# Performance work log

Measured on AMD Instinct MI355X. Metric: run time of the kernel, lower is better.

Reference implementation:

```python
import jax, jax.numpy as jnp
import numpy as np
import math

H = 16
D_MODEL = 1024
D_K = D_MODEL // H  # 64
B = 4
S = 2048
D_V = 64


def setup_inputs() -> dict:
    key0 = jax.random.key(0)
    ks = jax.random.split(key0, 7)
    scale = 1.0 / math.sqrt(D_MODEL)
    return {
        "query": jax.random.normal(ks[0], (B, S, D_MODEL), jnp.float32),
        "key": jax.random.normal(ks[1], (B, S, D_MODEL), jnp.float32),
        "value": jax.random.normal(ks[2], (B, D_V, S), jnp.float32),
        "Wq": jax.random.normal(ks[3], (D_MODEL, D_MODEL), jnp.float32) * scale,
        "bq": jax.random.normal(ks[4], (D_MODEL,), jnp.float32) * scale,
        "Wk": jax.random.normal(ks[5], (D_MODEL, D_MODEL), jnp.float32) * scale,
        "bk": jax.random.normal(ks[6], (D_MODEL,), jnp.float32) * scale,
    }


def reference(query, key, value, Wq, bq, Wk, bk):
    nb = query.shape[0]
    # Linear projections then split heads: [B,S,d_model] -> [B,h,S,d_k]
    q = (query @ Wq.T + bq).reshape(nb, -1, H, D_K).transpose(0, 2, 1, 3)
    k = (key @ Wk.T + bk).reshape(nb, -1, H, D_K).transpose(0, 2, 1, 3)
    # value.repeat(h,1,1,1).permute(1,0,3,2): [B,dv,Sk] -> broadcast over heads
    # with last two axes swapped -> effectively v[b,s,d] = value[b,d,s]
    v = jnp.swapaxes(value, 1, 2)  # [B, Sk, dv]
    # Scaled dot-product attention (mask branch is a no-op: m == zeros)
    scores = jnp.einsum("bhqd,bhkd->bhqk", q, k) / math.sqrt(D_K)
    p_attn = jax.nn.softmax(scores, axis=-1)
    # value identical across heads, contract directly with base v
    x = jnp.einsum("bhqk,bkd->bhqd", p_attn, v)  # [B,h,Sq,dv]
    return (jnp.mean(x, axis=1), q)
```

## Files before the change

### kernel.cpp

```cpp
#include <hip/hip_runtime.h>


typedef unsigned short u16;
typedef __attribute__((ext_vector_type(8))) u16 u16x8;
typedef __attribute__((ext_vector_type(8))) __bf16 bf16x8;
typedef __attribute__((ext_vector_type(4))) float f32x4;
typedef __attribute__((ext_vector_type(16))) float f32x16;
typedef __attribute__((ext_vector_type(2))) unsigned u32x2;
typedef __attribute__((ext_vector_type(4))) unsigned u32x4;

typedef const __attribute__((address_space(1))) void gvoid;
typedef __attribute__((address_space(3))) void lvoid;

__device__ __forceinline__ void gload16(const void* g, void* l) {
  __builtin_amdgcn_global_load_lds((gvoid*)g, (lvoid*)l, 16, 0, 0);
}

__device__ __forceinline__ u16 f2bf(float f) {
  unsigned u = __builtin_bit_cast(unsigned, f);
  u += 0x7fffu + ((u >> 16) & 1u);
  return (u16)(u >> 16);
}

__device__ __forceinline__ unsigned cvtpk(float lo, float hi) {
  unsigned r;
  asm("v_cvt_pk_bf16_f32 %0, %1, %2" : "=v"(r) : "v"(lo), "v"(hi));
  return r;
}

__device__ __forceinline__ float exp2a(float x) {
  float r;
  asm("v_exp_f32 %0, %1" : "=v"(r) : "v"(x));
  return r;
}

__device__ __forceinline__ f32x16 zero16() {
  f32x16 z;
#pragma unroll
  for (int i = 0; i < 16; ++i) z[i] = 0.f;
  return z;
}

__global__ void cvt_small(const float* __restrict__ wq, const float* __restrict__ wk,
                          const float* __restrict__ v,
                          u16* __restrict__ wqb, u16* __restrict__ wkb, u16* __restrict__ vb) {
  int i = blockIdx.x * 256 + threadIdx.x;
  const float* s;
  u16* d;
  int off;
  if (i < 262144)      { s = wq; d = wqb; off = i; }
  else if (i < 524288) { s = wk; d = wkb; off = i - 262144; }
  else if (i < 655360) { s = v;  d = vb;  off = i - 524288; }
  else return;
  float4 x = reinterpret_cast<const float4*>(s)[off];
  ushort4 o;
  o.x = f2bf(x.x); o.y = f2bf(x.y); o.z = f2bf(x.z); o.w = f2bf(x.w);
  reinterpret_cast<ushort4*>(d)[off] = o;
}

__global__ __launch_bounds__(256) void proj_gemm(
    const float* __restrict__ qf, const float* __restrict__ kf,
    const u16* __restrict__ Wqb, const u16* __restrict__ Wkb,
    const float* __restrict__ bq, const float* __restrict__ bk,
    float* __restrict__ out1, u16* __restrict__ k_ws)
{
  const int z = blockIdx.z;
  const float* __restrict__ A = z ? kf : qf;
  const u16* __restrict__ W = z ? Wkb : Wqb;
  const float* __restrict__ bias = z ? bk : bq;

  __shared__ u16 As[128 * 64];
  __shared__ u16 Bs[128 * 64];

  const int tid = threadIdx.x;
  const int lane = tid & 63;
  const int w = tid >> 6;
  const int ln = lane & 15;
  const int lh = lane >> 4;
  const int wm = w >> 1, wn = w & 1;
  const int n0 = blockIdx.x * 128;
  const int j0 = blockIdx.y * 128;

  f32x4 acc[4][4];
#pragma unroll
  for (int mt = 0; mt < 4; ++mt)
#pragma unroll
    for (int nt = 0; nt < 4; ++nt)
      acc[mt][nt] = f32x4{0.f, 0.f, 0.f, 0.f};

  const int r_ = tid >> 3, c8_ = tid & 7;

  for (int kt = 0; kt < 16; ++kt) {
    __syncthreads();
#pragma unroll
    for (int it = 0; it < 4; ++it) {
      int r = it * 32 + r_;
      gload16(&W[(size_t)(j0 + r) * 1024 + kt * 64 + c8_ * 8], &Bs[(it * 256 + w * 64) * 8]);
    }
#pragma unroll
    for (int j = 0; j < 4; ++j) {
      int u = tid + j * 256;
      int r = u >> 3, c8 = (u & 7) * 8;
      const float* s = &A[(size_t)(n0 + r) * 1024 + kt * 64 + c8];
      float4 x0 = *reinterpret_cast<const float4*>(s);
      float4 x1 = *reinterpret_cast<const float4*>(s + 4);
      u32x4 wv{cvtpk(x0.x, x0.y), cvtpk(x0.z, x0.w), cvtpk(x1.x, x1.y), cvtpk(x1.z, x1.w)};
      *reinterpret_cast<u32x4*>(&As[r * 64 + c8]) = wv;
    }
    __syncthreads();
#pragma unroll
    for (int ks = 0; ks < 2; ++ks) {
      bf16x8 a[4], bfr[4];
#pragma unroll
      for (int mt = 0; mt < 4; ++mt)
        a[mt] = __builtin_bit_cast(bf16x8,
            *reinterpret_cast<const u16x8*>(&As[(wm * 64 + mt * 16 + ln) * 64 + lh * 8 + ks * 32]));
#pragma unroll
      for (int nt = 0; nt < 4; ++nt)
        bfr[nt] = __builtin_bit_cast(bf16x8,
            *reinterpret_cast<const u16x8*>(&Bs[(wn * 64 + nt * 16 + ln) * 64 + lh * 8 + ks * 32]));
      __builtin_amdgcn_s_setprio(1);
#pragma unroll
      for (int mt = 0; mt < 4; ++mt)
#pragma unroll
        for (int nt = 0; nt < 4; ++nt)
          acc[mt][nt] = __builtin_amdgcn_mfma_f32_16x16x32_bf16(a[mt], bfr[nt], acc[mt][nt], 0, 0, 0);
      __builtin_amdgcn_s_setprio(0);
    }
  }

#pragma unroll
  for (int nt = 0; nt < 4; ++nt) {
    int j = j0 + wn * 64 + nt * 16 + ln;
    float bv = bias[j];
    int h = j >> 6, d = j & 63;
#pragma unroll
    for (int mt = 0; mt < 4; ++mt) {
#pragma unroll
      for (int r = 0; r < 4; ++r) {
        int n = n0 + wm * 64 + mt * 16 + lh * 4 + r;
        int bidx = n >> 11, s = n & 2047;
        size_t off = ((size_t)(bidx * 16 + h) * 2048 + s) * 64 + d;
        float val = acc[mt][nt][r] + bv;
        if (z == 0) out1[off] = val;
        else        k_ws[off] = f2bf(val);
      }
    }
  }
}

__global__ __launch_bounds__(256) void attn_kernel(
    const float* __restrict__ qf, const u16* __restrict__ k_ws,
    const u16* __restrict__ valb, float* __restrict__ x_ws)
{
  const int wgid = (blockIdx.x & 7) * 128 + (blockIdx.x >> 3);
  const int qblk = wgid & 15;
  const int h = (wgid >> 4) & 15;
  const int b = wgid >> 8;
  const int bh = b * 16 + h;

  const int tid = threadIdx.x, lane = tid & 63, w = tid >> 6;
  const int l31 = lane & 31, hi = lane >> 5;
  const int xm = (lane & 7) << 4;

  __shared__ u16 Kt[2][4096];
  __shared__ u16 Vt[2][4096];
  char* KtB = (char*)&Kt[0][0];
  char* VtB = (char*)&Vt[0][0];

  bf16x8 aq[4];
  {
    const float qs = 0.125f * 1.4426950408889634f;
    const size_t qbase = ((size_t)bh * 2048 + qblk * 128 + w * 32 + l31) * 64;
#pragma unroll
    for (int c = 0; c < 4; ++c) {
      float4 v0 = *reinterpret_cast<const float4*>(&qf[qbase + c * 16 + hi * 8]);
      float4 v1 = *reinterpret_cast<const float4*>(&qf[qbase + c * 16 + hi * 8 + 4]);
      u16x8 t;
      t[0] = f2bf(v0.x * qs); t[1] = f2bf(v0.y * qs);
      t[2] = f2bf(v0.z * qs); t[3] = f2bf(v0.w * qs);
      t[4] = f2bf(v1.x * qs); t[5] = f2bf(v1.y * qs);
      t[6] = f2bf(v1.z * qs); t[7] = f2bf(v1.w * qs);
      aq[c] = __builtin_bit_cast(bf16x8, t);
    }
  }

  const u16* kg = k_ws + (size_t)bh * 131072;
  const u16* vg = valb + (size_t)b * 131072;
  const int u0 = tid, u1 = tid + 256;
  const u16* ks0 = kg + (u0 >> 3) * 64 + ((u0 ^ (u0 >> 3)) & 7) * 8;
  const u16* ks1 = kg + (u1 >> 3) * 64 + ((u1 ^ (u1 >> 3)) & 7) * 8;
  const u16* vs0 = vg + (u0 >> 3) * 2048 + ((u0 ^ (u0 >> 3)) & 7) * 8;
  const u16* vs1 = vg + (u1 >> 3) * 2048 + ((u1 ^ (u1 >> 3)) & 7) * 8;
  u16* kd0 = &Kt[0][(w * 64) * 8];
  u16* kd1 = &Kt[0][(256 + w * 64) * 8];
  u16* vd0 = &Vt[0][(w * 64) * 8];
  u16* vd1 = &Vt[0][(256 + w * 64) * 8];

  gload16(ks0, kd0); gload16(ks1, kd1);
  gload16(vs0, vd0); gload16(vs1, vd1);

  float l_loc = 0.0f;
  f32x16 oA = zero16(), oB = zero16();
  int cur = 0;
  __syncthreads();

  for (int t = 0; t < 32; ++t) {
    if (t < 31) {
      int nb = (cur ^ 1) * 4096;
      size_t ko = (size_t)(t + 1) * 4096;
      int vo = (t + 1) * 64;
      gload16(ks0 + ko, kd0 + nb); gload16(ks1 + ko, kd1 + nb);
      gload16(vs0 + vo, vd0 + nb); gload16(vs1 + vo, vd1 + nb);
    }
    const int bo = cur * 8192;

#pragma unroll
    for (int st = 0; st < 2; ++st) {
      f32x16 p = zero16();
      __builtin_amdgcn_s_setprio(1);
#pragma unroll
      for (int c = 0; c < 4; ++c) {
        int kaddr = bo + ((((st * 32 + l31) * 128) + c * 32 + hi * 16) ^ xm);
        bf16x8 kf = __builtin_bit_cast(bf16x8, *reinterpret_cast<const u16x8*>(KtB + kaddr));
        p = __builtin_amdgcn_mfma_f32_32x32x16_bf16(kf, aq[c], p, 0, 0, 0);
      }
      __builtin_amdgcn_s_setprio(0);

#pragma unroll
      for (int r = 0; r < 16; ++r) p[r] = exp2a(p[r]);
      float s0 = (p[0] + p[1]) + (p[2] + p[3]);
      float s1 = (p[4] + p[5]) + (p[6] + p[7]);
      float s2 = (p[8] + p[9]) + (p[10] + p[11]);
      float s3 = (p[12] + p[13]) + (p[14] + p[15]);
      l_loc += (s0 + s1) + (s2 + s3);

      u32x2 sA0 = __builtin_amdgcn_permlane32_swap(cvtpk(p[0], p[1]),   cvtpk(p[4], p[5]),   false, false);
      u32x2 sB0 = __builtin_amdgcn_permlane32_swap(cvtpk(p[2], p[3]),   cvtpk(p[6], p[7]),   false, false);
      u32x2 sA1 = __builtin_amdgcn_permlane32_swap(cvtpk(p[8], p[9]),   cvtpk(p[12], p[13]), false, false);
      u32x2 sB1 = __builtin_amdgcn_permlane32_swap(cvtpk(p[10], p[11]), cvtpk(p[14], p[15]), false, false);
      u32x4 w0{sA0[0], sB0[0], sA0[1], sB0[1]};
      u32x4 w1{sA1[0], sB1[0], sA1[1], sB1[1]};
      bf16x8 pf0 = __builtin_bit_cast(bf16x8, w0);
      bf16x8 pf1 = __builtin_bit_cast(bf16x8, w1);

#pragma unroll
      for (int kc = 0; kc < 2; ++kc) {
        bf16x8 pf = kc ? pf1 : pf0;
        int cb = st * 64 + kc * 32 + hi * 16;
        bf16x8 vA = __builtin_bit_cast(bf16x8,
            *reinterpret_cast<const u16x8*>(VtB + bo + ((l31 * 128 + cb) ^ xm)));
        bf16x8 vB = __builtin_bit_cast(bf16x8,
            *reinterpret_cast<const u16x8*>(VtB + bo + (((32 + l31) * 128 + cb) ^ xm)));
        __builtin_amdgcn_s_setprio(1);
        oA = __builtin_amdgcn_mfma_f32_32x32x16_bf16(vA, pf, oA, 0, 0, 0);
        oB = __builtin_amdgcn_mfma_f32_32x32x16_bf16(vB, pf, oB, 0, 0, 0);
        __builtin_amdgcn_s_setprio(0);
      }
    }
    __syncthreads();
    cur ^= 1;
  }

  float l_run = l_loc + __shfl_xor(l_loc, 32);
  float inv = 1.0f / l_run;
  size_t obase = ((size_t)bh * 2048 + qblk * 128 + w * 32 + l31) * 64;
#pragma unroll
  for (int g = 0; g < 4; ++g) {
    float4 aa, bb;
    aa.x = oA[g * 4 + 0] * inv; aa.y = oA[g * 4 + 1] * inv;
    aa.z = oA[g * 4 + 2] * inv; aa.w = oA[g * 4 + 3] * inv;
    bb.x = oB[g * 4 + 0] * inv; bb.y = oB[g * 4 + 1] * inv;
    bb.z = oB[g * 4 + 2] * inv; bb.w = oB[g * 4 + 3] * inv;
    *reinterpret_cast<float4*>(&x_ws[obase + g * 8 + hi * 4]) = aa;
    *reinterpret_cast<float4*>(&x_ws[obase + 32 + g * 8 + hi * 4]) = bb;
  }
}

__global__ void mean_heads(const float* __restrict__ x_ws, float* __restrict__ out0) {
  int idx = blockIdx.x * 256 + threadIdx.x;
  int b = idx >> 17;
  int rem = idx & 131071;
  float s = 0.f;
#pragma unroll
  for (int h = 0; h < 16; ++h) s += x_ws[((size_t)(b * 16 + h) << 17) + rem];
  out0[idx] = s * 0.0625f;
}

extern "C" void kernel_launch(void* const* d_in, const int* in_sizes, int n_in,
                              void* d_out, int out_size, void* d_ws, size_t ws_size,
                              hipStream_t stream) {
  (void)in_sizes; (void)n_in; (void)out_size; (void)ws_size;
  const float* query = (const float*)d_in[0];
  const float* key   = (const float*)d_in[1];
  const float* value = (const float*)d_in[2];
  const float* Wq    = (const float*)d_in[3];
  const float* bq    = (const float*)d_in[4];
  const float* Wk    = (const float*)d_in[5];
  const float* bk    = (const float*)d_in[6];

  float* out0 = (float*)d_out;
  float* out1 = out0 + 524288;

  char* ws = (char*)d_ws;
  const size_t MB = 1u << 20;
  u16* Wqb  = (u16*)(ws + 32 * MB);
  u16* Wkb  = (u16*)(ws + 34 * MB);
  u16* valb = (u16*)(ws + 36 * MB);
  u16* k_ws = (u16*)(ws + 37 * MB);
  float* x_ws = (float*)(ws + 0);

  cvt_small<<<2560, 256, 0, stream>>>(Wq, Wk, value, Wqb, Wkb, valb);
  proj_gemm<<<dim3(64, 8, 2), 256, 0, stream>>>(query, key, Wqb, Wkb, bq, bk, out1, k_ws);
  attn_kernel<<<1024, 256, 0, stream>>>(out1, k_ws, valb, x_ws);
  mean_heads<<<2048, 256, 0, stream>>>(x_ws, out0);
}
```

Baseline: 175.0 us.

## Double attention workgroup to 512 threads with 256 queries sharing each K/V tile

The attention kernel now launches 512 workgroups of 8 waves, each covering 256 query rows, so every K/V tile staged in LDS is reused by twice as many waves. Each thread issues one async global-to-LDS load per tensor instead of two. The inner loop also computes both QK^T score tiles before running the softmax and PV MMAs, giving the scheduler more independent work. The cost is fewer workgroups, register pressure from holding two score tiles under the 512-thread launch bound, and barriers that now synchronise twice as many waves.

```diff
diff --git a/kernel.cpp b/kernel.cpp
--- a/kernel.cpp
+++ b/kernel.cpp
@@ -149,14 +149,30 @@
   }
 }
 
-__global__ __launch_bounds__(256) void attn_kernel(
+#define SOFTMAX_CVT(P, PF0, PF1)                                                     \
+  {                                                                                  \
+    _Pragma("unroll")                                                                \
+    for (int r = 0; r < 16; ++r) P[r] = exp2a(P[r]);                                 \
+    l_loc += (((P[0]+P[1])+(P[2]+P[3])) + ((P[4]+P[5])+(P[6]+P[7])))                 \
+           + (((P[8]+P[9])+(P[10]+P[11])) + ((P[12]+P[13])+(P[14]+P[15])));          \
+    u32x2 sA0 = __builtin_amdgcn_permlane32_swap(cvtpk(P[0],P[1]),   cvtpk(P[4],P[5]),   false,false); \
+    u32x2 sB0 = __builtin_amdgcn_permlane32_swap(cvtpk(P[2],P[3]),   cvtpk(P[6],P[7]),   false,false); \
+    u32x2 sA1 = __builtin_amdgcn_permlane32_swap(cvtpk(P[8],P[9]),   cvtpk(P[12],P[13]), false,false); \
+    u32x2 sB1 = __builtin_amdgcn_permlane32_swap(cvtpk(P[10],P[11]), cvtpk(P[14],P[15]), false,false); \
+    u32x4 w0_{sA0[0], sB0[0], sA0[1], sB0[1]};                                       \
+    u32x4 w1_{sA1[0], sB1[0], sA1[1], sB1[1]};                                       \
+    PF0 = __builtin_bit_cast(bf16x8, w0_);                                           \
+    PF1 = __builtin_bit_cast(bf16x8, w1_);                                           \
+  }
+
+__global__ __launch_bounds__(512) void attn_kernel(
     const float* __restrict__ qf, const u16* __restrict__ k_ws,
     const u16* __restrict__ valb, float* __restrict__ x_ws)
 {
-  const int wgid = (blockIdx.x & 7) * 128 + (blockIdx.x >> 3);
-  const int qblk = wgid & 15;
-  const int h = (wgid >> 4) & 15;
-  const int b = wgid >> 8;
+  const int wgid = (blockIdx.x & 7) * 64 + (blockIdx.x >> 3);
+  const int qblk = wgid & 7;
+  const int h = (wgid >> 3) & 15;
+  const int b = wgid >> 7;
   const int bh = b * 16 + h;
 
   const int tid = threadIdx.x, lane = tid & 63, w = tid >> 6;
@@ -171,7 +187,7 @@
   bf16x8 aq[4];
   {
     const float qs = 0.125f * 1.4426950408889634f;
-    const size_t qbase = ((size_t)bh * 2048 + qblk * 128 + w * 32 + l31) * 64;
+    const size_t qbase = ((size_t)bh * 2048 + qblk * 256 + w * 32 + l31) * 64;
 #pragma unroll
     for (int c = 0; c < 4; ++c) {
       float4 v0 = *reinterpret_cast<const float4*>(&qf[qbase + c * 16 + hi * 8]);
@@ -187,18 +203,13 @@
 
   const u16* kg = k_ws + (size_t)bh * 131072;
   const u16* vg = valb + (size_t)b * 131072;
-  const int u0 = tid, u1 = tid + 256;
-  const u16* ks0 = kg + (u0 >> 3) * 64 + ((u0 ^ (u0 >> 3)) & 7) * 8;
-  const u16* ks1 = kg + (u1 >> 3) * 64 + ((u1 ^ (u1 >> 3)) & 7) * 8;
-  const u16* vs0 = vg + (u0 >> 3) * 2048 + ((u0 ^ (u0 >> 3)) & 7) * 8;
-  const u16* vs1 = vg + (u1 >> 3) * 2048 + ((u1 ^ (u1 >> 3)) & 7) * 8;
-  u16* kd0 = &Kt[0][(w * 64) * 8];
-  u16* kd1 = &Kt[0][(256 + w * 64) * 8];
-  u16* vd0 = &Vt[0][(w * 64) * 8];
-  u16* vd1 = &Vt[0][(256 + w * 64) * 8];
-
-  gload16(ks0, kd0); gload16(ks1, kd1);
-  gload16(vs0, vd0); gload16(vs1, vd1);
+  const u16* ksA = kg + (tid >> 3) * 64 + ((tid ^ (tid >> 3)) & 7) * 8;
+  const u16* vsA = vg + (tid >> 3) * 2048 + ((tid ^ (tid >> 3)) & 7) * 8;
+  u16* kdA = &Kt[0][w * 512];
+  u16* vdA = &Vt[0][w * 512];
+
+  gload16(ksA, kdA);
+  gload16(vsA, vdA);
 
   float l_loc = 0.0f;
   f32x16 oA = zero16(), oB = zero16();
@@ -208,63 +219,73 @@
   for (int t = 0; t < 32; ++t) {
     if (t < 31) {
       int nb = (cur ^ 1) * 4096;
-      size_t ko = (size_t)(t + 1) * 4096;
-      int vo = (t + 1) * 64;
-      gload16(ks0 + ko, kd0 + nb); gload16(ks1 + ko, kd1 + nb);
-      gload16(vs0 + vo, vd0 + nb); gload16(vs1 + vo, vd1 + nb);
+      gload16(ksA + (size_t)(t + 1) * 4096, kdA + nb);
+      gload16(vsA + (t + 1) * 64, vdA + nb);
     }
     const int bo = cur * 8192;
 
-#pragma unroll
-    for (int st = 0; st < 2; ++st) {
-      f32x16 p = zero16();
+    f32x16 p0 = zero16(), p1 = zero16();
+    __builtin_amdgcn_s_setprio(1);
+#pragma unroll
+    for (int c = 0; c < 4; ++c) {
+      int ka = bo + (((l31 * 128) + c * 32 + hi * 16) ^ xm);
+      bf16x8 kf = __builtin_bit_cast(bf16x8, *reinterpret_cast<const u16x8*>(KtB + ka));
+      p0 = __builtin_amdgcn_mfma_f32_32x32x16_bf16(kf, aq[c], p0, 0, 0, 0);
+    }
+#pragma unroll
+    for (int c = 0; c < 4; ++c) {
+      int ka = bo + ((((32 + l31) * 128) + c * 32 + hi * 16) ^ xm);
+      bf16x8 kf = __builtin_bit_cast(bf16x8, *reinterpret_cast<const u16x8*>(KtB + ka));
+      p1 = __builtin_amdgcn_mfma_f32_32x32x16_bf16(kf, aq[c], p1, 0, 0, 0);
+    }
+    __builtin_amdgcn_s_setprio(0);
+
+    bf16x8 pf00, pf01, pf10, pf11;
+    SOFTMAX_CVT(p0, pf00, pf01);
+
+    {
+      bf16x8 vA0 = __builtin_bit_cast(bf16x8,
+          *reinterpret_cast<const u16x8*>(VtB + bo + ((l31 * 128 + 0 * 32 + hi * 16) ^ xm)));
+      bf16x8 vB0 = __builtin_bit_cast(bf16x8,
+          *reinterpret_cast<const u16x8*>(VtB + bo + (((32 + l31) * 128 + 0 * 32 + hi * 16) ^ xm)));
+      bf16x8 vA1 = __builtin_bit_cast(bf16x8,
+          *reinterpret_cast<const u16x8*>(VtB + bo + ((l31 * 128 + 1 * 32 + hi * 16) ^ xm)));
+      bf16x8 vB1 = __builtin_bit_cast(bf16x8,
+          *reinterpret_cast<const u16x8*>(VtB + bo + (((32 + l31) * 128 + 1 * 32 + hi * 16) ^ xm)));
       __builtin_amdgcn_s_setprio(1);
-#pragma unroll
-      for (int c = 0; c < 4; ++c) {
-        int kaddr = bo + ((((st * 32 + l31) * 128) + c * 32 + hi * 16) ^ xm);
-        bf16x8 kf = __builtin_bit_cast(bf16x8, *reinterpret_cast<const u16x8*>(KtB + kaddr));
-        p = __builtin_amdgcn_mfma_f32_32x32x16_bf16(kf, aq[c], p, 0, 0, 0);
-      }
+      oA = __builtin_amdgcn_mfma_f32_32x32x16_bf16(vA0, pf00, oA, 0, 0, 0);
+      oB = __builtin_amdgcn_mfma_f32_32x32x16_bf16(vB0, pf00, oB, 0, 0, 0);
+      oA = __builtin_amdgcn_mfma_f32_32x32x16_bf16(vA1, pf01, oA, 0, 0, 0);
+      oB = __builtin_amdgcn_mfma_f32_32x32x16_bf16(vB1, pf01, oB, 0, 0, 0);
       __builtin_amdgcn_s_setprio(0);
-
-#pragma unroll
-      for (int r = 0; r < 16; ++r) p[r] = exp2a(p[r]);
-      float s0 = (p[0] + p[1]) + (p[2] + p[3]);
-      float s1 = (p[4] + p[5]) + (p[6] + p[7]);
-      float s2 = (p[8] + p[9]) + (p[10] + p[11]);
-      float s3 = (p[12] + p[13]) + (p[14] + p[15]);
-      l_loc += (s0 + s1) + (s2 + s3);
-
-      u32x2 sA0 = __builtin_amdgcn_permlane32_swap(cvtpk(p[0], p[1]),   cvtpk(p[4], p[5]),   false, false);
-      u32x2 sB0 = __builtin_amdgcn_permlane32_swap(cvtpk(p[2], p[3]),   cvtpk(p[6], p[7]),   false, false);
-      u32x2 sA1 = __builtin_amdgcn_permlane32_swap(cvtpk(p[8], p[9]),   cvtpk(p[12], p[13]), false, false);
-      u32x2 sB1 = __builtin_amdgcn_permlane32_swap(cvtpk(p[10], p[11]), cvtpk(p[14], p[15]), false, false);
-      u32x4 w0{sA0[0], sB0[0], sA0[1], sB0[1]};
-      u32x4 w1{sA1[0], sB1[0], sA1[1], sB1[1]};
-      bf16x8 pf0 = __builtin_bit_cast(bf16x8, w0);
-      bf16x8 pf1 = __builtin_bit_cast(bf16x8, w1);
-
-#pragma unroll
-      for (int kc = 0; kc < 2; ++kc) {
-        bf16x8 pf = kc ? pf1 : pf0;
-        int cb = st * 64 + kc * 32 + hi * 16;
-        bf16x8 vA = __builtin_bit_cast(bf16x8,
-            *reinterpret_cast<const u16x8*>(VtB + bo + ((l31 * 128 + cb) ^ xm)));
-        bf16x8 vB = __builtin_bit_cast(bf16x8,
-            *reinterpret_cast<const u16x8*>(VtB + bo + (((32 + l31) * 128 + cb) ^ xm)));
-        __builtin_amdgcn_s_setprio(1);
-        oA = __builtin_amdgcn_mfma_f32_32x32x16_bf16(vA, pf, oA, 0, 0, 0);
-        oB = __builtin_amdgcn_mfma_f32_32x32x16_bf16(vB, pf, oB, 0, 0, 0);
-        __builtin_amdgcn_s_setprio(0);
-      }
-    }
+    }
+
+    SOFTMAX_CVT(p1, pf10, pf11);
+
+    {
+      bf16x8 vA0 = __builtin_bit_cast(bf16x8,
+          *reinterpret_cast<const u16x8*>(VtB + bo + ((l31 * 128 + 64 + 0 * 32 + hi * 16) ^ xm)));
+      bf16x8 vB0 = __builtin_bit_cast(bf16x8,
+          *reinterpret_cast<const u16x8*>(VtB + bo + (((32 + l31) * 128 + 64 + 0 * 32 + hi * 16) ^ xm)));
+      bf16x8 vA1 = __builtin_bit_cast(bf16x8,
+          *reinterpret_cast<const u16x8*>(VtB + bo + ((l31 * 128 + 64 + 1 * 32 + hi * 16) ^ xm)));
+      bf16x8 vB1 = __builtin_bit_cast(bf16x8,
+          *reinterpret_cast<const u16x8*>(VtB + bo + (((32 + l31) * 128 + 64 + 1 * 32 + hi * 16) ^ xm)));
+      __builtin_amdgcn_s_setprio(1);
+      oA = __builtin_amdgcn_mfma_f32_32x32x16_bf16(vA0, pf10, oA, 0, 0, 0);
+      oB = __builtin_amdgcn_mfma_f32_32x32x16_bf16(vB0, pf10, oB, 0, 0, 0);
+      oA = __builtin_amdgcn_mfma_f32_32x32x16_bf16(vA1, pf11, oA, 0, 0, 0);
+      oB = __builtin_amdgcn_mfma_f32_32x32x16_bf16(vB1, pf11, oB, 0, 0, 0);
+      __builtin_amdgcn_s_setprio(0);
+    }
+
     __syncthreads();
     cur ^= 1;
   }
 
   float l_run = l_loc + __shfl_xor(l_loc, 32);
   float inv = 1.0f / l_run;
-  size_t obase = ((size_t)bh * 2048 + qblk * 128 + w * 32 + l31) * 64;
+  size_t obase = ((size_t)bh * 2048 + qblk * 256 + w * 32 + l31) * 64;
 #pragma unroll
   for (int g = 0; g < 4; ++g) {
     float4 aa, bb;
@@ -312,6 +333,6 @@
 
   cvt_small<<<2560, 256, 0, stream>>>(Wq, Wk, value, Wqb, Wkb, valb);
   proj_gemm<<<dim3(64, 8, 2), 256, 0, stream>>>(query, key, Wqb, Wkb, bq, bk, out1, k_ws);
-  attn_kernel<<<1024, 256, 0, stream>>>(out1, k_ws, valb, x_ws);
+  attn_kernel<<<512, 512, 0, stream>>>(out1, k_ws, valb, x_ws);
   mean_heads<<<2048, 256, 0, stream>>>(x_ws, out0);
 }
```

After: 173.0 us. About the same (-1.1%).

## Double query rows per wave in attention and store bf16 head outputs

Applied to the files above, without the earlier changes.

Each wave now processes 64 query rows as two 32-row groups, so every K and V fragment read from LDS feeds two MFMAs. This halves the LDS traffic and K/V tile loads per query row, and the attention grid shrinks to 512 blocks. The per-head attention output is now stored as bf16 instead of fp32, and mean_heads reads 8-wide vectors, cutting workspace traffic. The costs are more registers for the doubled accumulators, fewer workgroups to spread across CUs, and lower precision in the intermediate head outputs.

```diff
diff --git a/kernel.cpp b/kernel.cpp
--- a/kernel.cpp
+++ b/kernel.cpp
@@ -149,14 +149,63 @@
   }
 }
 
+#define SOFTMAX_CVT(P, PF0, PF1, LACC)                                               \
+  {                                                                                  \
+    _Pragma("unroll")                                                                \
+    for (int r = 0; r < 16; ++r) P[r] = exp2a(P[r]);                                 \
+    LACC += (((P[0]+P[1])+(P[2]+P[3])) + ((P[4]+P[5])+(P[6]+P[7])))                  \
+          + (((P[8]+P[9])+(P[10]+P[11])) + ((P[12]+P[13])+(P[14]+P[15])));           \
+    u32x2 sA0 = __builtin_amdgcn_permlane32_swap(cvtpk(P[0],P[1]),   cvtpk(P[4],P[5]),   false,false); \
+    u32x2 sB0 = __builtin_amdgcn_permlane32_swap(cvtpk(P[2],P[3]),   cvtpk(P[6],P[7]),   false,false); \
+    u32x2 sA1 = __builtin_amdgcn_permlane32_swap(cvtpk(P[8],P[9]),   cvtpk(P[12],P[13]), false,false); \
+    u32x2 sB1 = __builtin_amdgcn_permlane32_swap(cvtpk(P[10],P[11]), cvtpk(P[14],P[15]), false,false); \
+    u32x4 w0_{sA0[0], sB0[0], sA0[1], sB0[1]};                                       \
+    u32x4 w1_{sA1[0], sB1[0], sA1[1], sB1[1]};                                       \
+    PF0 = __builtin_bit_cast(bf16x8, w0_);                                           \
+    PF1 = __builtin_bit_cast(bf16x8, w1_);                                           \
+  }
+
+#define ST_BLOCK(ST)                                                                 \
+  {                                                                                  \
+    f32x16 pA = zero16(), pB = zero16();                                             \
+    __builtin_amdgcn_s_setprio(1);                                                   \
+    _Pragma("unroll")                                                                \
+    for (int c = 0; c < 4; ++c) {                                                    \
+      int ka = bo + ((((ST * 32 + l31) * 128) + c * 32 + hi * 16) ^ xm);             \
+      bf16x8 kf = __builtin_bit_cast(bf16x8, *reinterpret_cast<const u16x8*>(KtB + ka)); \
+      pA = __builtin_amdgcn_mfma_f32_32x32x16_bf16(kf, aqA[c], pA, 0, 0, 0);         \
+      pB = __builtin_amdgcn_mfma_f32_32x32x16_bf16(kf, aqB[c], pB, 0, 0, 0);         \
+    }                                                                                \
+    __builtin_amdgcn_s_setprio(0);                                                   \
+    bf16x8 fA0, fA1, fB0, fB1;                                                       \
+    SOFTMAX_CVT(pA, fA0, fA1, lA);                                                   \
+    SOFTMAX_CVT(pB, fB0, fB1, lB);                                                   \
+    _Pragma("unroll")                                                                \
+    for (int kc = 0; kc < 2; ++kc) {                                                 \
+      int cb = ST * 64 + kc * 32 + hi * 16;                                          \
+      bf16x8 vA = __builtin_bit_cast(bf16x8,                                         \
+          *reinterpret_cast<const u16x8*>(VtB + bo + ((l31 * 128 + cb) ^ xm)));      \
+      bf16x8 vB = __builtin_bit_cast(bf16x8,                                         \
+          *reinterpret_cast<const u16x8*>(VtB + bo + (((32 + l31) * 128 + cb) ^ xm))); \
+      bf16x8 fA = kc ? fA1 : fA0;                                                    \
+      bf16x8 fB = kc ? fB1 : fB0;                                                    \
+      __builtin_amdgcn_s_setprio(1);                                                 \
+      oA0 = __builtin_amdgcn_mfma_f32_32x32x16_bf16(vA, fA, oA0, 0, 0, 0);           \
+      oB0 = __builtin_amdgcn_mfma_f32_32x32x16_bf16(vB, fA, oB0, 0, 0, 0);           \
+      oA1 = __builtin_amdgcn_mfma_f32_32x32x16_bf16(vA, fB, oA1, 0, 0, 0);           \
+      oB1 = __builtin_amdgcn_mfma_f32_32x32x16_bf16(vB, fB, oB1, 0, 0, 0);           \
+      __builtin_amdgcn_s_setprio(0);                                                 \
+    }                                                                                \
+  }
+
 __global__ __launch_bounds__(256) void attn_kernel(
     const float* __restrict__ qf, const u16* __restrict__ k_ws,
-    const u16* __restrict__ valb, float* __restrict__ x_ws)
+    const u16* __restrict__ valb, u16* __restrict__ x_ws)
 {
-  const int wgid = (blockIdx.x & 7) * 128 + (blockIdx.x >> 3);
-  const int qblk = wgid & 15;
-  const int h = (wgid >> 4) & 15;
-  const int b = wgid >> 8;
+  const int wgid = (blockIdx.x & 7) * 64 + (blockIdx.x >> 3);
+  const int qblk = wgid & 7;
+  const int h = (wgid >> 3) & 15;
+  const int b = wgid >> 7;
   const int bh = b * 16 + h;
 
   const int tid = threadIdx.x, lane = tid & 63, w = tid >> 6;
@@ -168,20 +217,26 @@
   char* KtB = (char*)&Kt[0][0];
   char* VtB = (char*)&Vt[0][0];
 
-  bf16x8 aq[4];
+  bf16x8 aqA[4], aqB[4];
   {
     const float qs = 0.125f * 1.4426950408889634f;
-    const size_t qbase = ((size_t)bh * 2048 + qblk * 128 + w * 32 + l31) * 64;
+    const size_t qb0 = ((size_t)bh * 2048 + qblk * 256 + w * 64 + l31) * 64;
+    const size_t qb1 = qb0 + (size_t)32 * 64;
 #pragma unroll
     for (int c = 0; c < 4; ++c) {
-      float4 v0 = *reinterpret_cast<const float4*>(&qf[qbase + c * 16 + hi * 8]);
-      float4 v1 = *reinterpret_cast<const float4*>(&qf[qbase + c * 16 + hi * 8 + 4]);
-      u16x8 t;
-      t[0] = f2bf(v0.x * qs); t[1] = f2bf(v0.y * qs);
-      t[2] = f2bf(v0.z * qs); t[3] = f2bf(v0.w * qs);
-      t[4] = f2bf(v1.x * qs); t[5] = f2bf(v1.y * qs);
-      t[6] = f2bf(v1.z * qs); t[7] = f2bf(v1.w * qs);
-      aq[c] = __builtin_bit_cast(bf16x8, t);
+#pragma unroll
+      for (int g = 0; g < 2; ++g) {
+        const float* src = g ? &qf[qb1 + c * 16 + hi * 8] : &qf[qb0 + c * 16 + hi * 8];
+        float4 v0 = *reinterpret_cast<const float4*>(src);
+        float4 v1 = *reinterpret_cast<const float4*>(src + 4);
+        u16x8 t;
+        t[0] = f2bf(v0.x * qs); t[1] = f2bf(v0.y * qs);
+        t[2] = f2bf(v0.z * qs); t[3] = f2bf(v0.w * qs);
+        t[4] = f2bf(v1.x * qs); t[5] = f2bf(v1.y * qs);
+        t[6] = f2bf(v1.z * qs); t[7] = f2bf(v1.w * qs);
+        if (g) aqB[c] = __builtin_bit_cast(bf16x8, t);
+        else   aqA[c] = __builtin_bit_cast(bf16x8, t);
+      }
     }
   }
 
@@ -200,8 +255,8 @@
   gload16(ks0, kd0); gload16(ks1, kd1);
   gload16(vs0, vd0); gload16(vs1, vd1);
 
-  float l_loc = 0.0f;
-  f32x16 oA = zero16(), oB = zero16();
+  float lA = 0.0f, lB = 0.0f;
+  f32x16 oA0 = zero16(), oB0 = zero16(), oA1 = zero16(), oB1 = zero16();
   int cur = 0;
   __syncthreads();
 
@@ -215,76 +270,52 @@
     }
     const int bo = cur * 8192;
 
-#pragma unroll
-    for (int st = 0; st < 2; ++st) {
-      f32x16 p = zero16();
-      __builtin_amdgcn_s_setprio(1);
-#pragma unroll
-      for (int c = 0; c < 4; ++c) {
-        int kaddr = bo + ((((st * 32 + l31) * 128) + c * 32 + hi * 16) ^ xm);
-        bf16x8 kf = __builtin_bit_cast(bf16x8, *reinterpret_cast<const u16x8*>(KtB + kaddr));
-        p = __builtin_amdgcn_mfma_f32_32x32x16_bf16(kf, aq[c], p, 0, 0, 0);
-      }
-      __builtin_amdgcn_s_setprio(0);
-
-#pragma unroll
-      for (int r = 0; r < 16; ++r) p[r] = exp2a(p[r]);
-      float s0 = (p[0] + p[1]) + (p[2] + p[3]);
-      float s1 = (p[4] + p[5]) + (p[6] + p[7]);
-      float s2 = (p[8] + p[9]) + (p[10] + p[11]);
-      float s3 = (p[12] + p[13]) + (p[14] + p[15]);
-      l_loc += (s0 + s1) + (s2 + s3);
-
-      u32x2 sA0 = __builtin_amdgcn_permlane32_swap(cvtpk(p[0], p[1]),   cvtpk(p[4], p[5]),   false, false);
-      u32x2 sB0 = __builtin_amdgcn_permlane32_swap(cvtpk(p[2], p[3]),   cvtpk(p[6], p[7]),   false, false);
-      u32x2 sA1 = __builtin_amdgcn_permlane32_swap(cvtpk(p[8], p[9]),   cvtpk(p[12], p[13]), false, false);
-      u32x2 sB1 = __builtin_amdgcn_permlane32_swap(cvtpk(p[10], p[11]), cvtpk(p[14], p[15]), false, false);
-      u32x4 w0{sA0[0], sB0[0], sA0[1], sB0[1]};
-      u32x4 w1{sA1[0], sB1[0], sA1[1], sB1[1]};
-      bf16x8 pf0 = __builtin_bit_cast(bf16x8, w0);
-      bf16x8 pf1 = __builtin_bit_cast(bf16x8, w1);
-
-#pragma unroll
-      for (int kc = 0; kc < 2; ++kc) {
-        bf16x8 pf = kc ? pf1 : pf0;
-        int cb = st * 64 + kc * 32 + hi * 16;
-        bf16x8 vA = __builtin_bit_cast(bf16x8,
-            *reinterpret_cast<const u16x8*>(VtB + bo + ((l31 * 128 + cb) ^ xm)));
-        bf16x8 vB = __builtin_bit_cast(bf16x8,
-            *reinterpret_cast<const u16x8*>(VtB + bo + (((32 + l31) * 128 + cb) ^ xm)));
-        __builtin_amdgcn_s_setprio(1);
-        oA = __builtin_amdgcn_mfma_f32_32x32x16_bf16(vA, pf, oA, 0, 0, 0);
-        oB = __builtin_amdgcn_mfma_f32_32x32x16_bf16(vB, pf, oB, 0, 0, 0);
-        __builtin_amdgcn_s_setprio(0);
-      }
-    }
+    ST_BLOCK(0)
+    ST_BLOCK(1)
+
     __syncthreads();
     cur ^= 1;
   }
 
-  float l_run = l_loc + __shfl_xor(l_loc, 32);
-  float inv = 1.0f / l_run;
-  size_t obase = ((size_t)bh * 2048 + qblk * 128 + w * 32 + l31) * 64;
+  float lrA = lA + __shfl_xor(lA, 32);
+  float lrB = lB + __shfl_xor(lB, 32);
+  float invA = 1.0f / lrA, invB = 1.0f / lrB;
+  size_t ob0 = ((size_t)bh * 2048 + qblk * 256 + w * 64 + l31) * 64;
+  size_t ob1 = ob0 + (size_t)32 * 64;
 #pragma unroll
   for (int g = 0; g < 4; ++g) {
-    float4 aa, bb;
-    aa.x = oA[g * 4 + 0] * inv; aa.y = oA[g * 4 + 1] * inv;
-    aa.z = oA[g * 4 + 2] * inv; aa.w = oA[g * 4 + 3] * inv;
-    bb.x = oB[g * 4 + 0] * inv; bb.y = oB[g * 4 + 1] * inv;
-    bb.z = oB[g * 4 + 2] * inv; bb.w = oB[g * 4 + 3] * inv;
-    *reinterpret_cast<float4*>(&x_ws[obase + g * 8 + hi * 4]) = aa;
-    *reinterpret_cast<float4*>(&x_ws[obase + 32 + g * 8 + hi * 4]) = bb;
-  }
-}
-
-__global__ void mean_heads(const float* __restrict__ x_ws, float* __restrict__ out0) {
-  int idx = blockIdx.x * 256 + threadIdx.x;
-  int b = idx >> 17;
-  int rem = idx & 131071;
-  float s = 0.f;
-#pragma unroll
-  for (int h = 0; h < 16; ++h) s += x_ws[((size_t)(b * 16 + h) << 17) + rem];
-  out0[idx] = s * 0.0625f;
+    u32x2 aa{cvtpk(oA0[g*4+0]*invA, oA0[g*4+1]*invA), cvtpk(oA0[g*4+2]*invA, oA0[g*4+3]*invA)};
+    u32x2 bb{cvtpk(oB0[g*4+0]*invA, oB0[g*4+1]*invA), cvtpk(oB0[g*4+2]*invA, oB0[g*4+3]*invA)};
+    u32x2 cc{cvtpk(oA1[g*4+0]*invB, oA1[g*4+1]*invB), cvtpk(oA1[g*4+2]*invB, oA1[g*4+3]*invB)};
+    u32x2 dd{cvtpk(oB1[g*4+0]*invB, oB1[g*4+1]*invB), cvtpk(oB1[g*4+2]*invB, oB1[g*4+3]*invB)};
+    *reinterpret_cast<u32x2*>(&x_ws[ob0 + g * 8 + hi * 4]) = aa;
+    *reinterpret_cast<u32x2*>(&x_ws[ob0 + 32 + g * 8 + hi * 4]) = bb;
+    *reinterpret_cast<u32x2*>(&x_ws[ob1 + g * 8 + hi * 4]) = cc;
+    *reinterpret_cast<u32x2*>(&x_ws[ob1 + 32 + g * 8 + hi * 4]) = dd;
+  }
+}
+
+__global__ void mean_heads(const u16* __restrict__ x_ws, float* __restrict__ out0) {
+  int i = blockIdx.x * 256 + threadIdx.x;
+  int d0 = (i & 7) * 8;
+  int s = (i >> 3) & 2047;
+  int b = i >> 14;
+  float acc[8];
+#pragma unroll
+  for (int j = 0; j < 8; ++j) acc[j] = 0.f;
+#pragma unroll
+  for (int h = 0; h < 16; ++h) {
+    u16x8 v = *reinterpret_cast<const u16x8*>(
+        &x_ws[(((size_t)(b * 16 + h) * 2048 + s) << 6) + d0]);
+#pragma unroll
+    for (int j = 0; j < 8; ++j)
+      acc[j] += __builtin_bit_cast(float, (unsigned)v[j] << 16);
+  }
+  float4 o0{acc[0] * 0.0625f, acc[1] * 0.0625f, acc[2] * 0.0625f, acc[3] * 0.0625f};
+  float4 o1{acc[4] * 0.0625f, acc[5] * 0.0625f, acc[6] * 0.0625f, acc[7] * 0.0625f};
+  size_t ob = ((size_t)(b * 2048 + s) << 6) + d0;
+  *reinterpret_cast<float4*>(&out0[ob]) = o0;
+  *reinterpret_cast<float4*>(&out0[ob + 4]) = o1;
 }
 
 extern "C" void kernel_launch(void* const* d_in, const int* in_sizes, int n_in,
@@ -308,10 +339,10 @@
   u16* Wkb  = (u16*)(ws + 34 * MB);
   u16* valb = (u16*)(ws + 36 * MB);
   u16* k_ws = (u16*)(ws + 37 * MB);
-  float* x_ws = (float*)(ws + 0);
+  u16* x_ws = (u16*)(ws + 0);
 
   cvt_small<<<2560, 256, 0, stream>>>(Wq, Wk, value, Wqb, Wkb, valb);
   proj_gemm<<<dim3(64, 8, 2), 256, 0, stream>>>(query, key, Wqb, Wkb, bq, bk, out1, k_ws);
-  attn_kernel<<<1024, 256, 0, stream>>>(out1, k_ws, valb, x_ws);
-  mean_heads<<<2048, 256, 0, stream>>>(x_ws, out0);
-}
+  attn_kernel<<<512, 256, 0, stream>>>(out1, k_ws, valb, x_ws);
+  mean_heads<<<256, 256, 0, stream>>>(x_ws, out0);
+}
```

New measurement: 164.0 us. 6.3% less time.
